# Performance work log

Measured on AMD Instinct MI355X. Metric: run time of the kernel, lower is better.

The kernel has to match this reference:

```python
import jax, jax.numpy as jnp
import numpy as np

KH, KW = 3, 3
H_OUT, W_OUT = 62, 62

def setup_inputs() -> dict:
    key = jax.random.key(0)
    k1, k2 = jax.random.split(key)
    x = jax.random.normal(k1, (16, 32, 64, 64), dtype=jnp.float32)
    weight = jax.random.normal(k2, (H_OUT, W_OUT, 64, 32, KH, KW), dtype=jnp.float32) * 0.01
    return {"x": x, "weight": weight}

def reference(x, weight):
    # Unfold: patches[b,c,kh,kw,i,j] = x[b,c,i+kh,j+kw]; small fixed 3x3 loop is fine.
    patches = jnp.stack([
        jnp.stack([x[:, :, kh:kh + H_OUT, kw:kw + W_OUT] for kw in range(KW)], axis=2)
        for kh in range(KH)
    ], axis=2)  # [B, C_in, kH, kW, H_out, W_out]
    # Per-position (no weight sharing) contraction over c_in, kh, kw.
    out = jnp.einsum('bcklij,ijockl->boij', patches, weight)
    return jax.nn.sigmoid(out)
```

## Files before the change

kernel.cpp:

```cpp
#include <hip/hip_runtime.h>

#define HO 62
#define WO 62
#define CIN 32
#define COUT 64
#define BATCH 16
#define KROW 288
#define JT 4
#define COLS 6

typedef float f4a4 __attribute__((ext_vector_type(4), aligned(4)));

__global__ __launch_bounds__(256, 4)
void lc2d_kernel(const float* __restrict__ x,
                 const float* __restrict__ wgt,
                 float* __restrict__ out) {
    __shared__ __align__(16) float win[CIN][3][COLS][BATCH];

    const int blk = blockIdx.x;
    const int i  = blk % HO;
    const int j0 = (blk / HO) * JT;

    const int t = threadIdx.x;

    for (int r = t; r < BATCH * CIN * 3; r += 256) {
        const int b   = r & 15;
        const int ckh = r >> 4;
        const int c   = ckh / 3;
        const int kh  = ckh % 3;
        const float* src = x + (((b * CIN + c) * 64) + (i + kh)) * 64;
        #pragma unroll
        for (int cc = 0; cc < COLS; cc++) {
            int col = j0 + cc;
            if (col > 63) col = 63;
            win[c][kh][cc][b] = src[col];
        }
    }
    __syncthreads();

    const int wsel = t >> 6;
    const int o    = t & 63;

    const float* wj[JT];
    #pragma unroll
    for (int jj = 0; jj < JT; jj++) {
        int pj = i * WO + (j0 + jj);
        if (pj > HO * WO - 1) pj = HO * WO - 1;
        wj[jj] = wgt + (size_t)pj * (COUT * KROW) + o * KROW;
    }

    float acc[JT][4];
    #pragma unroll
    for (int jj = 0; jj < JT; jj++)
        #pragma unroll
        for (int bb = 0; bb < 4; bb++) acc[jj][bb] = 0.0f;

    const float* xbase = &win[0][0][0][wsel * 4];

    for (int c = 0; c < CIN; c++) {
        float wq[JT][9];
        #pragma unroll
        for (int jj = 0; jj < JT; jj++) {
            const float* p = wj[jj] + c * 9;
            const f4a4 wA = *(const f4a4*)p;
            const f4a4 wB = *(const f4a4*)(p + 4);
            wq[jj][0] = wA.x; wq[jj][1] = wA.y; wq[jj][2] = wA.z; wq[jj][3] = wA.w;
            wq[jj][4] = wB.x; wq[jj][5] = wB.y; wq[jj][6] = wB.z; wq[jj][7] = wB.w;
            wq[jj][8] = p[8];
        }
        #pragma unroll
        for (int kh = 0; kh < 3; kh++) {
            float4 xv[COLS];
            const float* xb = xbase + (c * 3 + kh) * (COLS * BATCH);
            #pragma unroll
            for (int cc = 0; cc < COLS; cc++)
                xv[cc] = *(const float4*)(xb + cc * BATCH);
            #pragma unroll
            for (int jj = 0; jj < JT; jj++) {
                #pragma unroll
                for (int kw = 0; kw < 3; kw++) {
                    const float w = wq[jj][kh * 3 + kw];
                    const float4 xx = xv[jj + kw];
                    acc[jj][0] += w * xx.x;
                    acc[jj][1] += w * xx.y;
                    acc[jj][2] += w * xx.z;
                    acc[jj][3] += w * xx.w;
                }
            }
        }
    }

    #pragma unroll
    for (int bb = 0; bb < 4; bb++) {
        const int b = wsel * 4 + bb;
        float* op = out + (((size_t)(b * COUT + o) * HO + i) * WO + j0);
        float2 s0;
        s0.x = 1.0f / (1.0f + __expf(-acc[0][bb]));
        s0.y = 1.0f / (1.0f + __expf(-acc[1][bb]));
        *(float2*)op = s0;
        if (j0 + 3 < WO) {
            float2 s1;
            s1.x = 1.0f / (1.0f + __expf(-acc[2][bb]));
            s1.y = 1.0f / (1.0f + __expf(-acc[3][bb]));
            *((float2*)op + 1) = s1;
        }
    }
}

extern "C" void kernel_launch(void* const* d_in, const int* in_sizes, int n_in,
                              void* d_out, int out_size, void* d_ws, size_t ws_size,
                              hipStream_t stream) {
    const float* x   = (const float*)d_in[0];
    const float* wgt = (const float*)d_in[1];
    float* out       = (float*)d_out;
    const int grid = HO * ((WO + JT - 1) / JT);
    lc2d_kernel<<<dim3(grid), dim3(256), 0, stream>>>(x, wgt, out);
}
```

Measured before the change: 571.7 us.

## Stage weights through double-buffered LDS with coalesced loads, shrink tile to two columns

Each phase of four input channels now has its weight slice loaded cooperatively and coalesced from global memory into padded LDS, using a register-staged double buffer with one barrier per phase. Previously each thread read its own strided 288-float weight row directly. The column tile drops from 4 to 2 positions per block, which doubles the grid and the redundant input-window loads, and launch bounds fall to 2 blocks per CU because of the larger LDS footprint. The kernel is bound by weight bandwidth, so the gain depends on better coalescing, traded against lower occupancy and extra synchronisation.

```diff
diff --git a/kernel.cpp b/kernel.cpp
--- a/kernel.cpp
+++ b/kernel.cpp
@@ -6,48 +6,65 @@
 #define COUT 64
 #define BATCH 16
 #define KROW 288
-#define JT 4
-#define COLS 6
+#define JT 2
+#define COLS 4
+#define ROWS 128
+#define PHASE_C 4
+#define PHASE_F (PHASE_C * 9)
+#define RSTRIDE 37
+#define NPHASE (CIN / PHASE_C)
 
-typedef float f4a4 __attribute__((ext_vector_type(4), aligned(4)));
-
-__global__ __launch_bounds__(256, 4)
+__global__ __launch_bounds__(256, 2)
 void lc2d_kernel(const float* __restrict__ x,
                  const float* __restrict__ wgt,
                  float* __restrict__ out) {
     __shared__ __align__(16) float win[CIN][3][COLS][BATCH];
+    __shared__ __align__(16) float wlds[2][ROWS * RSTRIDE];
 
     const int blk = blockIdx.x;
     const int i  = blk % HO;
     const int j0 = (blk / HO) * JT;
+    const int t  = threadIdx.x;
 
-    const int t = threadIdx.x;
+    int goffq[9], loffq[9];
+    #pragma unroll
+    for (int q = 0; q < 9; q++) {
+        const int f2  = q * 256 + t;
+        const int row = f2 / 18;
+        const int pos = f2 - row * 18;
+        goffq[q] = row * KROW + pos * 2;
+        loffq[q] = row * RSTRIDE + pos * 2;
+    }
 
-    for (int r = t; r < BATCH * CIN * 3; r += 256) {
-        const int b   = r & 15;
-        const int ckh = r >> 4;
-        const int c   = ckh / 3;
-        const int kh  = ckh % 3;
-        const float* src = x + (((b * CIN + c) * 64) + (i + kh)) * 64;
-        #pragma unroll
-        for (int cc = 0; cc < COLS; cc++) {
-            int col = j0 + cc;
-            if (col > 63) col = 63;
-            win[c][kh][cc][b] = src[col];
-        }
+    const float* wbase = wgt + (size_t)(i * WO + j0) * (COUT * KROW);
+
+    float2 stg[9];
+    #pragma unroll
+    for (int q = 0; q < 9; q++)
+        stg[q] = *(const float2*)(wbase + goffq[q]);
+
+    for (int r = t; r < BATCH * CIN * 3 * 2; r += 256) {
+        const int half = r & 1;
+        const int row  = r >> 1;
+        const int kh   = row % 3;
+        const int bc   = row / 3;
+        const int c    = bc & 31;
+        const int b    = bc >> 5;
+        const float2 v = *(const float2*)(x + (((b * CIN + c) * 64) + (i + kh)) * 64
+                                            + j0 + half * 2);
+        win[c][kh][half * 2][b]     = v.x;
+        win[c][kh][half * 2 + 1][b] = v.y;
+    }
+
+    #pragma unroll
+    for (int q = 0; q < 9; q++) {
+        wlds[0][loffq[q]]     = stg[q].x;
+        wlds[0][loffq[q] + 1] = stg[q].y;
     }
     __syncthreads();
 
     const int wsel = t >> 6;
     const int o    = t & 63;
-
-    const float* wj[JT];
-    #pragma unroll
-    for (int jj = 0; jj < JT; jj++) {
-        int pj = i * WO + (j0 + jj);
-        if (pj > HO * WO - 1) pj = HO * WO - 1;
-        wj[jj] = wgt + (size_t)pj * (COUT * KROW) + o * KROW;
-    }
 
     float acc[JT][4];
     #pragma unroll
@@ -56,54 +73,69 @@
         for (int bb = 0; bb < 4; bb++) acc[jj][bb] = 0.0f;
 
     const float* xbase = &win[0][0][0][wsel * 4];
+    const int wr0 = o * RSTRIDE;
 
-    for (int c = 0; c < CIN; c++) {
-        float wq[JT][9];
+    for (int p = 0; p < NPHASE; p++) {
+        const int cur = p & 1;
+
+        if (p < NPHASE - 1) {
+            const float* wp = wbase + (p + 1) * PHASE_F;
+            #pragma unroll
+            for (int q = 0; q < 9; q++)
+                stg[q] = *(const float2*)(wp + goffq[q]);
+        }
+
+        const float* wb = &wlds[cur][wr0];
         #pragma unroll
-        for (int jj = 0; jj < JT; jj++) {
-            const float* p = wj[jj] + c * 9;
-            const f4a4 wA = *(const f4a4*)p;
-            const f4a4 wB = *(const f4a4*)(p + 4);
-            wq[jj][0] = wA.x; wq[jj][1] = wA.y; wq[jj][2] = wA.z; wq[jj][3] = wA.w;
-            wq[jj][4] = wB.x; wq[jj][5] = wB.y; wq[jj][6] = wB.z; wq[jj][7] = wB.w;
-            wq[jj][8] = p[8];
-        }
-        #pragma unroll
-        for (int kh = 0; kh < 3; kh++) {
-            float4 xv[COLS];
-            const float* xb = xbase + (c * 3 + kh) * (COLS * BATCH);
-            #pragma unroll
-            for (int cc = 0; cc < COLS; cc++)
-                xv[cc] = *(const float4*)(xb + cc * BATCH);
+        for (int cc = 0; cc < PHASE_C; cc++) {
+            const int c = p * PHASE_C + cc;
+            float wq[JT][9];
             #pragma unroll
             for (int jj = 0; jj < JT; jj++) {
+                const float* wr = wb + jj * (64 * RSTRIDE) + cc * 9;
                 #pragma unroll
-                for (int kw = 0; kw < 3; kw++) {
-                    const float w = wq[jj][kh * 3 + kw];
-                    const float4 xx = xv[jj + kw];
-                    acc[jj][0] += w * xx.x;
-                    acc[jj][1] += w * xx.y;
-                    acc[jj][2] += w * xx.z;
-                    acc[jj][3] += w * xx.w;
+                for (int q = 0; q < 9; q++) wq[jj][q] = wr[q];
+            }
+            #pragma unroll
+            for (int kh = 0; kh < 3; kh++) {
+                float4 xv[COLS];
+                const float* xb = xbase + (c * 3 + kh) * (COLS * BATCH);
+                #pragma unroll
+                for (int cl = 0; cl < COLS; cl++)
+                    xv[cl] = *(const float4*)(xb + cl * BATCH);
+                #pragma unroll
+                for (int jj = 0; jj < JT; jj++) {
+                    #pragma unroll
+                    for (int kw = 0; kw < 3; kw++) {
+                        const float w  = wq[jj][kh * 3 + kw];
+                        const float4 xx = xv[jj + kw];
+                        acc[jj][0] += w * xx.x;
+                        acc[jj][1] += w * xx.y;
+                        acc[jj][2] += w * xx.z;
+                        acc[jj][3] += w * xx.w;
+                    }
                 }
             }
         }
+
+        if (p < NPHASE - 1) {
+            #pragma unroll
+            for (int q = 0; q < 9; q++) {
+                wlds[cur ^ 1][loffq[q]]     = stg[q].x;
+                wlds[cur ^ 1][loffq[q] + 1] = stg[q].y;
+            }
+        }
+        __syncthreads();
     }
 
     #pragma unroll
     for (int bb = 0; bb < 4; bb++) {
         const int b = wsel * 4 + bb;
         float* op = out + (((size_t)(b * COUT + o) * HO + i) * WO + j0);
-        float2 s0;
-        s0.x = 1.0f / (1.0f + __expf(-acc[0][bb]));
-        s0.y = 1.0f / (1.0f + __expf(-acc[1][bb]));
-        *(float2*)op = s0;
-        if (j0 + 3 < WO) {
-            float2 s1;
-            s1.x = 1.0f / (1.0f + __expf(-acc[2][bb]));
-            s1.y = 1.0f / (1.0f + __expf(-acc[3][bb]));
-            *((float2*)op + 1) = s1;
-        }
+        float2 s;
+        s.x = 1.0f / (1.0f + __expf(-acc[0][bb]));
+        s.y = 1.0f / (1.0f + __expf(-acc[1][bb]));
+        *(float2*)op = s;
     }
 }
 
@@ -113,6 +145,6 @@
     const float* x   = (const float*)d_in[0];
     const float* wgt = (const float*)d_in[1];
     float* out       = (float*)d_out;
-    const int grid = HO * ((WO + JT - 1) / JT);
+    const int grid = HO * (WO / JT);
     lc2d_kernel<<<dim3(grid), dim3(256), 0, stream>>>(x, wgt, out);
 }
```

Measured after the change: 482.6 us. -15.6%, faster.
